# Optimization experiments

Measured on AMD Instinct MI355X. Metric: run time of the kernel, lower is better.

Reference implementation:

```python
import jax, jax.numpy as jnp
import numpy as np

B, S, D = 2, 2048, 1024
E, N, HID = 8, 4, 4096

def setup_inputs() -> dict:
    key = jax.random.key(0)
    ks = jax.random.split(key, 6)
    x = jax.random.normal(ks[0], (B, S, D), dtype=jnp.float32)
    w_router = jax.random.normal(ks[1], (E, D), dtype=jnp.float32) * 0.02
    A_fc = jax.random.normal(ks[2], (E, N, N, N), dtype=jnp.float32) * 0.5
    S_fc = jax.random.normal(ks[3], (E, N, HID // N, D // N), dtype=jnp.float32) * (1.0 / np.sqrt(D))
    A_proj = jax.random.normal(ks[4], (E, N, N, N), dtype=jnp.float32) * 0.5
    S_proj = jax.random.normal(ks[5], (E, N, D // N, HID // N), dtype=jnp.float32) * (1.0 / np.sqrt(HID))
    return {"x": x, "w_router": w_router, "A_fc": A_fc, "S_fc": S_fc, "A_proj": A_proj, "S_proj": S_proj}

def _phm(Xn, A, S):
    # Xn: [T, n, s_in], S: [n, s_out, s_in], A: [n, n, n] -> [T, n, s_out]
    T_ = jnp.einsum('bkl,iol->bkio', Xn, S)
    return jnp.einsum('ijk,bkio->bjo', A, T_)

def reference(x, w_router, A_fc, S_fc, A_proj, S_proj):
    e_num, n = A_fc.shape[0], A_fc.shape[1]
    d = x.shape[-1]
    flat = x.reshape(-1, d)                      # [T, D]
    T = flat.shape[0]
    logits = flat @ w_router.T                   # [T, E]
    probs = jax.nn.softmax(logits, axis=-1)
    expert_idx = jnp.argmax(logits, axis=-1)     # [T]
    tpe = jnp.zeros((e_num,), flat.dtype).at[expert_idx].add(1.0)
    frac = tpe / T
    aux_loss = jnp.sum(frac * probs.mean(axis=0)) * e_num
    Xn = flat.reshape(T, n, d // n)
    out = jnp.zeros_like(flat)
    for e in range(e_num):                        # small fixed expert loop
        h = _phm(Xn, A_fc[e], S_fc[e]).reshape(T, -1)   # [T, HID]
        h = jnp.where(h >= 0, h, 0.5 * h)               # leaky_relu slope 0.5
        Hn = (h * h).reshape(T, n, -1)
        y = _phm(Hn, A_proj[e], S_proj[e]).reshape(T, d)
        out = out + jnp.where((expert_idx == e)[:, None], y, jnp.zeros((), flat.dtype))
    return out.reshape(x.shape), aux_loss
```

## Files before the change

kernel.cpp:

```cpp
#include <hip/hip_runtime.h>
#include <hip/hip_bf16.h>


#define T_TOK 4096
#define DIM   1024
#define NEXP  8
#define HIDD  4096
#define SLOTS 5120

static constexpr size_t OFF_WFC   = 0;
static constexpr size_t OFF_WPROJ = 67108864ull;
static constexpr size_t OFF_XB    = 134217728ull;
static constexpr size_t OFF_H     = 144703488ull;
static constexpr size_t OFF_BSUM  = 186646528ull;
static constexpr size_t OFF_EIDX  = OFF_BSUM + 1024*8*8;
static constexpr size_t OFF_TOK   = OFF_EIDX + (size_t)T_TOK*4;
static constexpr size_t OFF_CNT   = OFF_TOK + (size_t)SLOTS*4;

typedef __attribute__((ext_vector_type(8))) short short8;
typedef __attribute__((ext_vector_type(4))) float f32x4;

static __device__ __forceinline__ ushort f2bf(float f) {
    __hip_bfloat16 h = __float2bfloat16(f);
    return __builtin_bit_cast(ushort, h);
}

static __device__ __forceinline__ void gload_lds16(const ushort* g, ushort* l) {
    __builtin_amdgcn_global_load_lds((const __attribute__((address_space(1))) void*)g,
                                     (__attribute__((address_space(3))) void*)l,
                                     16, 0, 0);
}

__global__ __launch_bounds__(256) void front_k(const float* __restrict__ x,
                                               const float* __restrict__ wr,
                                               double* __restrict__ bsum,
                                               int* __restrict__ eidx,
                                               ushort* __restrict__ xb,
                                               const float* __restrict__ Afc,
                                               const float* __restrict__ Sfc,
                                               ushort* __restrict__ Wfc)
{
    __shared__ double shp[4][8];
    __shared__ float Ash[64];
    int tid = threadIdx.x;
    if (blockIdx.x < 1024) {
        int w = tid >> 6, lane = tid & 63;
        int t = blockIdx.x * 4 + w;
        const float4* xr = (const float4*)(x + (size_t)t * DIM);
        float4 xv[4];
#pragma unroll
        for (int q = 0; q < 4; q++) xv[q] = xr[q * 64 + lane];
        ushort4* xo = (ushort4*)(xb + (size_t)t * DIM);
#pragma unroll
        for (int q = 0; q < 4; q++) {
            float4 v = xv[q];
            ushort4 bq;
            bq.x = f2bf(v.x); bq.y = f2bf(v.y); bq.z = f2bf(v.z); bq.w = f2bf(v.w);
            xo[q * 64 + lane] = bq;
        }
        double lg[8];
#pragma unroll
        for (int e = 0; e < 8; e++) {
            const float4* wv = (const float4*)(wr + (size_t)e * DIM);
            double s = 0.0;
#pragma unroll
            for (int q = 0; q < 4; q++) {
                float4 a = xv[q], b = wv[q * 64 + lane];
                s += (double)a.x * b.x + (double)a.y * b.y + (double)a.z * b.z + (double)a.w * b.w;
            }
#pragma unroll
            for (int d = 1; d < 64; d <<= 1) s += __shfl_xor(s, d);
            lg[e] = s;
        }
        double m = lg[0];
#pragma unroll
        for (int e = 1; e < 8; e++) m = lg[e] > m ? lg[e] : m;
        double ex[8], sum = 0.0;
#pragma unroll
        for (int e = 0; e < 8; e++) { ex[e] = exp(lg[e] - m); sum += ex[e]; }
        if (lane < 8) shp[w][lane] = ex[lane] / sum;
        if (lane == 0) {
            int am = 0; double bv = lg[0];
#pragma unroll
            for (int e = 1; e < 8; e++) if (lg[e] > bv) { bv = lg[e]; am = e; }
            eidx[t] = am;
        }
        __syncthreads();
        if (tid < 8)
            bsum[(size_t)blockIdx.x * 8 + tid] =
                shp[0][tid] + shp[1][tid] + shp[2][tid] + shp[3][tid];
    } else {
        int b2 = blockIdx.x - 1024;
        int e = b2 >> 10, o = b2 & 1023;
        if (tid < 64) Ash[tid] = Afc[e * 64 + tid];
        __syncthreads();
        float s0 = Sfc[((size_t)(e * 4 + 0) * 1024 + o) * 256 + tid];
        float s1 = Sfc[((size_t)(e * 4 + 1) * 1024 + o) * 256 + tid];
        float s2 = Sfc[((size_t)(e * 4 + 2) * 1024 + o) * 256 + tid];
        float s3 = Sfc[((size_t)(e * 4 + 3) * 1024 + o) * 256 + tid];
        size_t base = (size_t)e * 4194304ull;
#pragma unroll
        for (int j = 0; j < 4; j++)
#pragma unroll
            for (int k = 0; k < 4; k++) {
                float v = Ash[j * 4 + k] * s0 + Ash[16 + j * 4 + k] * s1 +
                          Ash[32 + j * 4 + k] * s2 + Ash[48 + j * 4 + k] * s3;
                Wfc[base + (size_t)(j * 1024 + o) * 1024 + k * 256 + tid] = f2bf(v);
            }
    }
}

__global__ __launch_bounds__(256) void plan_k(const double* __restrict__ bsum,
                                              const int* __restrict__ eidx,
                                              int* __restrict__ counts,
                                              int* __restrict__ offsets,
                                              int* __restrict__ tok,
                                              float* __restrict__ auxout)
{
    __shared__ int hist[256][8];
    __shared__ double red[256][8];
    __shared__ int offs[8];
    int tid = threadIdx.x;
    for (int i = tid; i < SLOTS; i += 256) tok[i] = -1;
    int base = tid * 16;
    int le[16];
    int lc[8] = {0,0,0,0,0,0,0,0};
#pragma unroll
    for (int j = 0; j < 16; j++) { le[j] = eidx[base + j]; lc[le[j]]++; }
#pragma unroll
    for (int e = 0; e < 8; e++) hist[tid][e] = lc[e];
    __syncthreads();
    for (int s = 1; s < 256; s <<= 1) {
        int v[8];
        if (tid >= s) {
#pragma unroll
            for (int e = 0; e < 8; e++) v[e] = hist[tid - s][e];
        }
        __syncthreads();
        if (tid >= s) {
#pragma unroll
            for (int e = 0; e < 8; e++) hist[tid][e] += v[e];
        }
        __syncthreads();
    }
    int myBase[8];
#pragma unroll
    for (int e = 0; e < 8; e++) myBase[e] = hist[tid][e] - lc[e];
    if (tid == 0) {
        int off = 0;
#pragma unroll
        for (int e = 0; e < 8; e++) {
            int c = hist[255][e];
            counts[e] = c;
            offsets[e] = off; offs[e] = off;
            off += (c + 127) & ~127;
        }
    }
    __syncthreads();
    int cur[8];
#pragma unroll
    for (int e = 0; e < 8; e++) cur[e] = myBase[e];
#pragma unroll
    for (int j = 0; j < 16; j++) {
        int e = le[j];
        tok[offs[e] + cur[e]++] = base + j;
    }
    double ps[8] = {0, 0, 0, 0, 0, 0, 0, 0};
    for (int b = tid; b < 1024; b += 256) {
#pragma unroll
        for (int e = 0; e < 8; e++) ps[e] += bsum[(size_t)b * 8 + e];
    }
#pragma unroll
    for (int e = 0; e < 8; e++) red[tid][e] = ps[e];
    __syncthreads();
    for (int s = 128; s > 0; s >>= 1) {
        if (tid < s) {
#pragma unroll
            for (int e = 0; e < 8; e++) red[tid][e] += red[tid + s][e];
        }
        __syncthreads();
    }
    if (tid == 0) {
        double aux = 0.0;
#pragma unroll
        for (int e = 0; e < 8; e++)
            aux += ((double)hist[255][e] / T_TOK) * (red[0][e] / T_TOK);
        auxout[0] = (float)(aux * NEXP);
    }
}

__global__ __launch_bounds__(256, 2) void mid_k(const ushort* __restrict__ xb,
                                                const ushort* __restrict__ Wfc,
                                                ushort* __restrict__ h,
                                                const int* __restrict__ counts,
                                                const int* __restrict__ offsets,
                                                const int* __restrict__ tok,
                                                const float* __restrict__ Apj,
                                                const float* __restrict__ Spj,
                                                ushort* __restrict__ Wpj)
{
    __shared__ __align__(16) ushort As[128 * 64];
    __shared__ __align__(16) ushort Bs[256 * 64];
    __shared__ float Ashf[64];
    int b = blockIdx.x;
    int tid = threadIdx.x;
    if (b >= 640) {
        int b2 = b - 640;
        int e = b2 >> 8, o = b2 & 255;
        if (tid < 64) Ashf[tid] = Apj[e * 64 + tid];
        __syncthreads();
        float s[4][4];
#pragma unroll
        for (int i = 0; i < 4; i++)
#pragma unroll
            for (int q = 0; q < 4; q++)
                s[i][q] = Spj[((size_t)(e * 4 + i) * 256 + o) * 1024 + q * 256 + tid];
        size_t base = (size_t)e * 4194304ull;
#pragma unroll
        for (int j = 0; j < 4; j++)
#pragma unroll
            for (int k = 0; k < 4; k++) {
                float a0 = Ashf[j * 4 + k], a1 = Ashf[16 + j * 4 + k];
                float a2 = Ashf[32 + j * 4 + k], a3 = Ashf[48 + j * 4 + k];
#pragma unroll
                for (int q = 0; q < 4; q++) {
                    float v = a0 * s[0][q] + a1 * s[1][q] + a2 * s[2][q] + a3 * s[3][q];
                    Wpj[base + (size_t)(j * 256 + o) * 4096 + k * 1024 + q * 256 + tid] = f2bf(v);
                }
            }
        return;
    }
    constexpr int KDIM = 1024;
    constexpr int NDIM = 4096;
    int r = b >> 3;
    int nb = (b & 7) * 2 + r / 40;
    int ms = r % 40;
    int e = -1, mt = 0, acct = 0;
#pragma unroll
    for (int i = 0; i < 8; i++) {
        int tiles = (counts[i] + 127) >> 7;
        if (e < 0 && ms < acct + tiles) { e = i; mt = ms - acct; }
        acct += tiles;
    }
    if (e < 0) return;
    int m_base = offsets[e] + mt * 128;
    int n_base = nb * 256;
    int w = tid >> 6, lane = tid & 63;
    int wm = w >> 1, wn = w & 1;
    const ushort* Bb = Wfc + (size_t)e * NDIM * KDIM + (size_t)n_base * KDIM;
    int lr = lane >> 3;
    int lcs = (((lane & 7) ^ lr) << 3);
    const ushort* arow[4];
#pragma unroll
    for (int i = 0; i < 4; i++) {
        int sl = m_base + i * 32 + w * 8 + lr;
        int rt = tok[sl]; if (rt < 0) rt = 0;
        arow[i] = xb + (size_t)rt * KDIM + lcs;
    }
    f32x4 acc[4][8];
#pragma unroll
    for (int i = 0; i < 4; i++)
#pragma unroll
        for (int j = 0; j < 8; j++) acc[i][j] = (f32x4){0.f, 0.f, 0.f, 0.f};

    for (int t = 0; t < KDIM / 64; t++) {
        int k0 = t * 64;
#pragma unroll
        for (int i = 0; i < 4; i++)
            gload_lds16(arow[i] + k0, &As[(i * 32 + w * 8) * 64]);
#pragma unroll
        for (int i = 0; i < 8; i++) {
            int r0 = i * 32 + w * 8;
            gload_lds16(Bb + (size_t)(r0 + lr) * KDIM + k0 + lcs, &Bs[r0 * 64]);
        }
        __syncthreads();
#pragma unroll
        for (int ks = 0; ks < 2; ks++) {
            short8 a[4], bfr[8];
            int ca = (((ks * 4 + (lane >> 4)) ^ (lane & 7)) << 3);
#pragma unroll
            for (int f = 0; f < 4; f++)
                a[f] = *(const short8*)&As[(wm * 64 + f * 16 + (lane & 15)) * 64 + ca];
#pragma unroll
            for (int f = 0; f < 8; f++)
                bfr[f] = *(const short8*)&Bs[(wn * 128 + f * 16 + (lane & 15)) * 64 + ca];
#pragma unroll
            for (int mf = 0; mf < 4; mf++)
#pragma unroll
                for (int nf = 0; nf < 8; nf++)
                    acc[mf][nf] = __builtin_amdgcn_mfma_f32_16x16x32_bf16(a[mf], bfr[nf], acc[mf][nf], 0, 0, 0);
        }
        __syncthreads();
    }

    int col0 = n_base + wn * 128;
    int row0 = wm * 64 + (lane >> 4) * 4;
#pragma unroll
    for (int mf = 0; mf < 4; mf++)
#pragma unroll
        for (int nf = 0; nf < 8; nf++) {
            int col = col0 + nf * 16 + (lane & 15);
#pragma unroll
            for (int rg = 0; rg < 4; rg++) {
                float v = acc[mf][nf][rg];
                v = v >= 0.f ? v : 0.5f * v;
                v = v * v;
                h[(size_t)(m_base + row0 + mf * 16 + rg) * NDIM + col] = f2bf(v);
            }
        }
}

__global__ __launch_bounds__(256, 2) void proj_k(const ushort* __restrict__ h,
                                                 const ushort* __restrict__ Wpj,
                                                 float* __restrict__ out,
                                                 const int* __restrict__ counts,
                                                 const int* __restrict__ offsets,
                                                 const int* __restrict__ tok)
{
    __shared__ __align__(16) ushort As[128 * 64];
    __shared__ __align__(16) ushort Bs[256 * 64];
    constexpr int KDIM = 4096;
    constexpr int NDIM = 1024;
    constexpr int KSUB = 2048;
    int b = blockIdx.x;
    int nb = (b & 7) >> 1;
    int split = b & 1;
    int ms = b >> 3;
    int e = -1, mt = 0, acct = 0;
#pragma unroll
    for (int i = 0; i < 8; i++) {
        int tiles = (counts[i] + 127) >> 7;
        if (e < 0 && ms < acct + tiles) { e = i; mt = ms - acct; }
        acct += tiles;
    }
    if (e < 0) return;
    int m_base = offsets[e] + mt * 128;
    int n_base = nb * 256;
    int tid = threadIdx.x, w = tid >> 6, lane = tid & 63;
    int wm = w >> 1, wn = w & 1;
    int lr = lane >> 3;
    int lcs = (((lane & 7) ^ lr) << 3);
    int kbase = split * KSUB;
    const ushort* Bb = Wpj + (size_t)e * NDIM * KDIM + (size_t)n_base * KDIM + kbase;
    const ushort* arow[4];
#pragma unroll
    for (int i = 0; i < 4; i++)
        arow[i] = h + (size_t)(m_base + i * 32 + w * 8 + lr) * KDIM + kbase + lcs;
    f32x4 acc[4][8];
#pragma unroll
    for (int i = 0; i < 4; i++)
#pragma unroll
        for (int j = 0; j < 8; j++) acc[i][j] = (f32x4){0.f, 0.f, 0.f, 0.f};

    for (int t = 0; t < KSUB / 64; t++) {
        int k0 = t * 64;
#pragma unroll
        for (int i = 0; i < 4; i++)
            gload_lds16(arow[i] + k0, &As[(i * 32 + w * 8) * 64]);
#pragma unroll
        for (int i = 0; i < 8; i++) {
            int r0 = i * 32 + w * 8;
            gload_lds16(Bb + (size_t)(r0 + lr) * KDIM + k0 + lcs, &Bs[r0 * 64]);
        }
        __syncthreads();
#pragma unroll
        for (int ks = 0; ks < 2; ks++) {
            short8 a[4], bfr[8];
            int ca = (((ks * 4 + (lane >> 4)) ^ (lane & 7)) << 3);
#pragma unroll
            for (int f = 0; f < 4; f++)
                a[f] = *(const short8*)&As[(wm * 64 + f * 16 + (lane & 15)) * 64 + ca];
#pragma unroll
            for (int f = 0; f < 8; f++)
                bfr[f] = *(const short8*)&Bs[(wn * 128 + f * 16 + (lane & 15)) * 64 + ca];
#pragma unroll
            for (int mf = 0; mf < 4; mf++)
#pragma unroll
                for (int nf = 0; nf < 8; nf++)
                    acc[mf][nf] = __builtin_amdgcn_mfma_f32_16x16x32_bf16(a[mf], bfr[nf], acc[mf][nf], 0, 0, 0);
        }
        __syncthreads();
    }

    int col0 = n_base + wn * 128;
    int row0 = wm * 64 + (lane >> 4) * 4;
    int limit = offsets[e] + counts[e];
#pragma unroll
    for (int mf = 0; mf < 4; mf++) {
        int tk[4]; bool vld[4];
#pragma unroll
        for (int rg = 0; rg < 4; rg++) {
            int slot = m_base + row0 + mf * 16 + rg;
            vld[rg] = slot < limit;
            tk[rg] = vld[rg] ? tok[slot] : 0;
        }
#pragma unroll
        for (int nf = 0; nf < 8; nf++) {
            int col = col0 + nf * 16 + (lane & 15);
#pragma unroll
            for (int rg = 0; rg < 4; rg++)
                if (vld[rg]) unsafeAtomicAdd(&out[(size_t)tk[rg] * NDIM + col], acc[mf][nf][rg]);
        }
    }
}

extern "C" void kernel_launch(void* const* d_in, const int* in_sizes, int n_in,
                              void* d_out, int out_size, void* d_ws, size_t ws_size,
                              hipStream_t stream)
{
    const float* x    = (const float*)d_in[0];
    const float* wr   = (const float*)d_in[1];
    const float* A_fc = (const float*)d_in[2];
    const float* S_fc = (const float*)d_in[3];
    const float* A_pj = (const float*)d_in[4];
    const float* S_pj = (const float*)d_in[5];
    float* out = (float*)d_out;
    char* ws = (char*)d_ws;

    ushort* Wfc   = (ushort*)(ws + OFF_WFC);
    ushort* Wpj   = (ushort*)(ws + OFF_WPROJ);
    ushort* xb    = (ushort*)(ws + OFF_XB);
    ushort* h     = (ushort*)(ws + OFF_H);
    double* bsum  = (double*)(ws + OFF_BSUM);
    int*    eidx  = (int*)(ws + OFF_EIDX);
    int*    tok   = (int*)(ws + OFF_TOK);
    int*    counts  = (int*)(ws + OFF_CNT);
    int*    offsets = counts + 16;

    hipMemsetAsync(out, 0, (size_t)T_TOK * DIM * sizeof(float), stream);
    front_k<<<1024 + 8192, 256, 0, stream>>>(x, wr, bsum, eidx, xb, A_fc, S_fc, Wfc);
    plan_k<<<1, 256, 0, stream>>>(bsum, eidx, counts, offsets, tok,
                                  out + (size_t)T_TOK * DIM);
    mid_k<<<640 + 2048, 256, 0, stream>>>(xb, Wfc, h, counts, offsets, tok,
                                          A_pj, S_pj, Wpj);
    proj_k<<<320, 256, 0, stream>>>(h, Wpj, out, counts, offsets, tok);
}
```

Measured before the change: 194.0 us.

## Replace atomic scatter in proj with split-K partial buffers plus reduce kernel

```diff
diff --git a/kernel.cpp b/kernel.cpp
--- a/kernel.cpp
+++ b/kernel.cpp
@@ -312,10 +312,9 @@
 
 __global__ __launch_bounds__(256, 2) void proj_k(const ushort* __restrict__ h,
                                                  const ushort* __restrict__ Wpj,
-                                                 float* __restrict__ out,
+                                                 float* __restrict__ Part,
                                                  const int* __restrict__ counts,
-                                                 const int* __restrict__ offsets,
-                                                 const int* __restrict__ tok)
+                                                 const int* __restrict__ offsets)
 {
     __shared__ __align__(16) ushort As[128 * 64];
     __shared__ __align__(16) ushort Bs[256 * 64];
@@ -382,26 +381,33 @@
         __syncthreads();
     }
 
+    float* P = Part + (size_t)split * SLOTS * NDIM;
     int col0 = n_base + wn * 128;
     int row0 = wm * 64 + (lane >> 4) * 4;
-    int limit = offsets[e] + counts[e];
-#pragma unroll
-    for (int mf = 0; mf < 4; mf++) {
-        int tk[4]; bool vld[4];
-#pragma unroll
-        for (int rg = 0; rg < 4; rg++) {
-            int slot = m_base + row0 + mf * 16 + rg;
-            vld[rg] = slot < limit;
-            tk[rg] = vld[rg] ? tok[slot] : 0;
-        }
+#pragma unroll
+    for (int mf = 0; mf < 4; mf++)
 #pragma unroll
         for (int nf = 0; nf < 8; nf++) {
             int col = col0 + nf * 16 + (lane & 15);
 #pragma unroll
             for (int rg = 0; rg < 4; rg++)
-                if (vld[rg]) unsafeAtomicAdd(&out[(size_t)tk[rg] * NDIM + col], acc[mf][nf][rg]);
-        }
-    }
+                P[(size_t)(m_base + row0 + mf * 16 + rg) * NDIM + col] = acc[mf][nf][rg];
+        }
+}
+
+__global__ __launch_bounds__(256) void reduce_k(const float* __restrict__ P,
+                                                const int* __restrict__ tok,
+                                                float* __restrict__ out)
+{
+    int slot = blockIdx.x;
+    int t = tok[slot];
+    if (t < 0) return;
+    const float4* p0 = (const float4*)(P + (size_t)slot * DIM);
+    const float4* p1 = (const float4*)(P + (size_t)(SLOTS + slot) * DIM);
+    float4* o = (float4*)(out + (size_t)t * DIM);
+    int i = threadIdx.x;
+    float4 a = p0[i], b = p1[i];
+    o[i] = (float4){a.x + b.x, a.y + b.y, a.z + b.z, a.w + b.w};
 }
 
 extern "C" void kernel_launch(void* const* d_in, const int* in_sizes, int n_in,
@@ -418,6 +424,7 @@
     char* ws = (char*)d_ws;
 
     ushort* Wfc   = (ushort*)(ws + OFF_WFC);
+    float*  Part  = (float*)(ws + OFF_WFC);
     ushort* Wpj   = (ushort*)(ws + OFF_WPROJ);
     ushort* xb    = (ushort*)(ws + OFF_XB);
     ushort* h     = (ushort*)(ws + OFF_H);
@@ -427,11 +434,11 @@
     int*    counts  = (int*)(ws + OFF_CNT);
     int*    offsets = counts + 16;
 
-    hipMemsetAsync(out, 0, (size_t)T_TOK * DIM * sizeof(float), stream);
     front_k<<<1024 + 8192, 256, 0, stream>>>(x, wr, bsum, eidx, xb, A_fc, S_fc, Wfc);
     plan_k<<<1, 256, 0, stream>>>(bsum, eidx, counts, offsets, tok,
                                   out + (size_t)T_TOK * DIM);
     mid_k<<<640 + 2048, 256, 0, stream>>>(xb, Wfc, h, counts, offsets, tok,
                                           A_pj, S_pj, Wpj);
-    proj_k<<<320, 256, 0, stream>>>(h, Wpj, out, counts, offsets, tok);
-}
+    proj_k<<<320, 256, 0, stream>>>(h, Wpj, Part, counts, offsets);
+    reduce_k<<<SLOTS, 256, 0, stream>>>(Part, tok, out);
+}
```

Measured after the change: 178.1 us. 8.2% less time.

## Split proj K four ways into partial buffers, add reduce kernel, vectorize weight builds

Applied to the files above, without the earlier changes.

```diff
diff --git a/kernel.cpp b/kernel.cpp
--- a/kernel.cpp
+++ b/kernel.cpp
@@ -25,6 +25,12 @@
     return __builtin_bit_cast(ushort, h);
 }
 
+static __device__ __forceinline__ ushort4 f4bf(float4 v) {
+    ushort4 b;
+    b.x = f2bf(v.x); b.y = f2bf(v.y); b.z = f2bf(v.z); b.w = f2bf(v.w);
+    return b;
+}
+
 static __device__ __forceinline__ void gload_lds16(const ushort* g, ushort* l) {
     __builtin_amdgcn_global_load_lds((const __attribute__((address_space(1))) void*)g,
                                      (__attribute__((address_space(3))) void*)l,
@@ -52,12 +58,7 @@
         for (int q = 0; q < 4; q++) xv[q] = xr[q * 64 + lane];
         ushort4* xo = (ushort4*)(xb + (size_t)t * DIM);
 #pragma unroll
-        for (int q = 0; q < 4; q++) {
-            float4 v = xv[q];
-            ushort4 bq;
-            bq.x = f2bf(v.x); bq.y = f2bf(v.y); bq.z = f2bf(v.z); bq.w = f2bf(v.w);
-            xo[q * 64 + lane] = bq;
-        }
+        for (int q = 0; q < 4; q++) xo[q * 64 + lane] = f4bf(xv[q]);
         double lg[8];
 #pragma unroll
         for (int e = 0; e < 8; e++) {
@@ -94,19 +95,23 @@
         int e = b2 >> 10, o = b2 & 1023;
         if (tid < 64) Ash[tid] = Afc[e * 64 + tid];
         __syncthreads();
-        float s0 = Sfc[((size_t)(e * 4 + 0) * 1024 + o) * 256 + tid];
-        float s1 = Sfc[((size_t)(e * 4 + 1) * 1024 + o) * 256 + tid];
-        float s2 = Sfc[((size_t)(e * 4 + 2) * 1024 + o) * 256 + tid];
-        float s3 = Sfc[((size_t)(e * 4 + 3) * 1024 + o) * 256 + tid];
+        int k = tid >> 6, lq = tid & 63;
+        float4 sv[4];
+#pragma unroll
+        for (int i = 0; i < 4; i++)
+            sv[i] = *(const float4*)&Sfc[((size_t)(e * 4 + i) * 1024 + o) * 256 + lq * 4];
         size_t base = (size_t)e * 4194304ull;
 #pragma unroll
-        for (int j = 0; j < 4; j++)
-#pragma unroll
-            for (int k = 0; k < 4; k++) {
-                float v = Ash[j * 4 + k] * s0 + Ash[16 + j * 4 + k] * s1 +
-                          Ash[32 + j * 4 + k] * s2 + Ash[48 + j * 4 + k] * s3;
-                Wfc[base + (size_t)(j * 1024 + o) * 1024 + k * 256 + tid] = f2bf(v);
-            }
+        for (int j = 0; j < 4; j++) {
+            float a0 = Ash[j * 4 + k], a1 = Ash[16 + j * 4 + k];
+            float a2 = Ash[32 + j * 4 + k], a3 = Ash[48 + j * 4 + k];
+            float4 v;
+            v.x = a0 * sv[0].x + a1 * sv[1].x + a2 * sv[2].x + a3 * sv[3].x;
+            v.y = a0 * sv[0].y + a1 * sv[1].y + a2 * sv[2].y + a3 * sv[3].y;
+            v.z = a0 * sv[0].z + a1 * sv[1].z + a2 * sv[2].z + a3 * sv[3].z;
+            v.w = a0 * sv[0].w + a1 * sv[1].w + a2 * sv[2].w + a3 * sv[3].w;
+            *(ushort4*)&Wfc[base + (size_t)(j * 1024 + o) * 1024 + k * 256 + lq * 4] = f4bf(v);
+        }
     }
 }
 
@@ -209,12 +214,10 @@
         int e = b2 >> 8, o = b2 & 255;
         if (tid < 64) Ashf[tid] = Apj[e * 64 + tid];
         __syncthreads();
-        float s[4][4];
+        float4 sv[4];
 #pragma unroll
         for (int i = 0; i < 4; i++)
-#pragma unroll
-            for (int q = 0; q < 4; q++)
-                s[i][q] = Spj[((size_t)(e * 4 + i) * 256 + o) * 1024 + q * 256 + tid];
+            sv[i] = *(const float4*)&Spj[((size_t)(e * 4 + i) * 256 + o) * 1024 + tid * 4];
         size_t base = (size_t)e * 4194304ull;
 #pragma unroll
         for (int j = 0; j < 4; j++)
@@ -222,11 +225,12 @@
             for (int k = 0; k < 4; k++) {
                 float a0 = Ashf[j * 4 + k], a1 = Ashf[16 + j * 4 + k];
                 float a2 = Ashf[32 + j * 4 + k], a3 = Ashf[48 + j * 4 + k];
-#pragma unroll
-                for (int q = 0; q < 4; q++) {
-                    float v = a0 * s[0][q] + a1 * s[1][q] + a2 * s[2][q] + a3 * s[3][q];
-                    Wpj[base + (size_t)(j * 256 + o) * 4096 + k * 1024 + q * 256 + tid] = f2bf(v);
-                }
+                float4 v;
+                v.x = a0 * sv[0].x + a1 * sv[1].x + a2 * sv[2].x + a3 * sv[3].x;
+                v.y = a0 * sv[0].y + a1 * sv[1].y + a2 * sv[2].y + a3 * sv[3].y;
+                v.z = a0 * sv[0].z + a1 * sv[1].z + a2 * sv[2].z + a3 * sv[3].z;
+                v.w = a0 * sv[0].w + a1 * sv[1].w + a2 * sv[2].w + a3 * sv[3].w;
+                *(ushort4*)&Wpj[base + (size_t)(j * 256 + o) * 4096 + k * 1024 + tid * 4] = f4bf(v);
             }
         return;
     }
@@ -312,7 +316,7 @@
 
 __global__ __launch_bounds__(256, 2) void proj_k(const ushort* __restrict__ h,
                                                  const ushort* __restrict__ Wpj,
-                                                 float* __restrict__ out,
+                                                 float* __restrict__ Part,
                                                  const int* __restrict__ counts,
                                                  const int* __restrict__ offsets,
                                                  const int* __restrict__ tok)
@@ -321,11 +325,13 @@
     __shared__ __align__(16) ushort Bs[256 * 64];
     constexpr int KDIM = 4096;
     constexpr int NDIM = 1024;
-    constexpr int KSUB = 2048;
+    constexpr int KSUB = 1024;
     int b = blockIdx.x;
-    int nb = (b & 7) >> 1;
-    int split = b & 1;
-    int ms = b >> 3;
+    int r = b >> 3;
+    int combo = (b & 7) * 2 + r / 40;
+    int nb = combo >> 2;
+    int split = combo & 3;
+    int ms = r % 40;
     int e = -1, mt = 0, acct = 0;
 #pragma unroll
     for (int i = 0; i < 8; i++) {
@@ -382,6 +388,7 @@
         __syncthreads();
     }
 
+    float* P = Part + (size_t)split * T_TOK * NDIM;
     int col0 = n_base + wn * 128;
     int row0 = wm * 64 + (lane >> 4) * 4;
     int limit = offsets[e] + counts[e];
@@ -399,9 +406,24 @@
             int col = col0 + nf * 16 + (lane & 15);
 #pragma unroll
             for (int rg = 0; rg < 4; rg++)
-                if (vld[rg]) unsafeAtomicAdd(&out[(size_t)tk[rg] * NDIM + col], acc[mf][nf][rg]);
-        }
-    }
+                if (vld[rg]) P[(size_t)tk[rg] * NDIM + col] = acc[mf][nf][rg];
+        }
+    }
+}
+
+__global__ __launch_bounds__(256) void reduce_k(const float* __restrict__ P,
+                                                float* __restrict__ out)
+{
+    int t = blockIdx.x;
+    int i = threadIdx.x;
+    const float4* p0 = (const float4*)(P + (size_t)t * DIM);
+    const float4* p1 = (const float4*)(P + (size_t)(T_TOK + t) * DIM);
+    const float4* p2 = (const float4*)(P + (size_t)(2 * T_TOK + t) * DIM);
+    const float4* p3 = (const float4*)(P + (size_t)(3 * T_TOK + t) * DIM);
+    float4 a = p0[i], b = p1[i], c = p2[i], d = p3[i];
+    float4* o = (float4*)(out + (size_t)t * DIM);
+    o[i] = (float4){a.x + b.x + c.x + d.x, a.y + b.y + c.y + d.y,
+                    a.z + b.z + c.z + d.z, a.w + b.w + c.w + d.w};
 }
 
 extern "C" void kernel_launch(void* const* d_in, const int* in_sizes, int n_in,
@@ -418,6 +440,7 @@
     char* ws = (char*)d_ws;
 
     ushort* Wfc   = (ushort*)(ws + OFF_WFC);
+    float*  Part  = (float*)(ws + OFF_WFC);
     ushort* Wpj   = (ushort*)(ws + OFF_WPROJ);
     ushort* xb    = (ushort*)(ws + OFF_XB);
     ushort* h     = (ushort*)(ws + OFF_H);
@@ -427,11 +450,11 @@
     int*    counts  = (int*)(ws + OFF_CNT);
     int*    offsets = counts + 16;
 
-    hipMemsetAsync(out, 0, (size_t)T_TOK * DIM * sizeof(float), stream);
     front_k<<<1024 + 8192, 256, 0, stream>>>(x, wr, bsum, eidx, xb, A_fc, S_fc, Wfc);
     plan_k<<<1, 256, 0, stream>>>(bsum, eidx, counts, offsets, tok,
                                   out + (size_t)T_TOK * DIM);
     mid_k<<<640 + 2048, 256, 0, stream>>>(xb, Wfc, h, counts, offsets, tok,
                                           A_pj, S_pj, Wpj);
-    proj_k<<<320, 256, 0, stream>>>(h, Wpj, out, counts, offsets, tok);
-}
+    proj_k<<<640, 256, 0, stream>>>(h, Wpj, Part, counts, offsets, tok);
+    reduce_k<<<T_TOK, 256, 0, stream>>>(Part, out);
+}
```

Result: faster. 182.9 us (-5.7%).
